# Kernel optimization log

Measured on AMD Instinct MI355X. Metric: run time of the kernel, lower is better.

The kernel has to match this reference:

```python
import jax, jax.numpy as jnp
import numpy as np

H = 200  # hidden size
D = 1    # input size
T = 8192 # sequence length


def setup_inputs() -> dict:
    key = jax.random.key(0)
    ks = jax.random.split(key, 11)
    s = 1.0 / np.sqrt(H)  # torch LSTM init scale
    u = lambda k, shape: jax.random.uniform(k, shape, jnp.float32, -s, s)
    return {
        "input_seq": jax.random.normal(ks[0], (T, D), jnp.float32),
        "W_ih0": u(ks[1], (4 * H, D)),
        "W_hh0": u(ks[2], (4 * H, H)),
        "b_ih0": u(ks[3], (4 * H,)),
        "b_hh0": u(ks[4], (4 * H,)),
        "W_ih1": u(ks[5], (4 * H, H)),
        "W_hh1": u(ks[6], (4 * H, H)),
        "b_ih1": u(ks[7], (4 * H,)),
        "b_hh1": u(ks[8], (4 * H,)),
        "W_out": u(ks[9], (D, H)),
        "b_out": u(ks[10], (D,)),
    }


def _cell(pre, h, c, Whh):
    # pre: [4H] = x @ W_ih.T + b_ih + b_hh already folded in
    g = pre + h @ Whh.T
    i, f, gg, o = jnp.split(g, 4)
    i = jax.nn.sigmoid(i)
    f = jax.nn.sigmoid(f)
    gg = jnp.tanh(gg)
    o = jax.nn.sigmoid(o)
    c = f * c + i * gg
    h = o * jnp.tanh(c)
    return h, c


def reference(input_seq, W_ih0, W_hh0, b_ih0, b_hh0,
              W_ih1, W_hh1, b_ih1, b_hh1, W_out, b_out):
    x = input_seq.reshape(input_seq.shape[0], -1)  # [T, D]
    # precompute layer-0 input projections for all timesteps (one big GEMM)
    pre0 = x @ W_ih0.T + (b_ih0 + b_hh0)           # [T, 4H]
    b1 = b_ih1 + b_hh1

    def step(carry, p0):
        h0, c0, h1, c1 = carry
        h0, c0 = _cell(p0, h0, c0, W_hh0)
        # eval mode: dropout(0.1) between layers is identity
        h1, c1 = _cell(h0 @ W_ih1.T + b1, h1, c1, W_hh1)
        return (h0, c0, h1, c1), None

    z = jnp.zeros((H,), x.dtype)
    (h0, c0, h1, c1), _ = jax.lax.scan(step, (z, z, z, z), pre0)
    # predictions[-1]: linear head on last top-layer hidden state -> [D]
    return h1 @ W_out.T + b_out
```

## Files before the change

### kernel.cpp

```cpp
#include <hip/hip_runtime.h>

#define TT 8192
#define HH 200
#define RD 1024
#define RDM 1023
#define BPWIN 900

typedef unsigned long long u64;
typedef unsigned int u32;
typedef _Float16 f16;
typedef _Float16 f16x2 __attribute__((ext_vector_type(2)));
typedef _Float16 half8 __attribute__((ext_vector_type(8)));
typedef float f32x4 __attribute__((ext_vector_type(4)));

__device__ __forceinline__ float sigmoidf_(float x){ return 1.0f/(1.0f+__expf(-x)); }
__device__ __forceinline__ float tanhf_(float x){
    float e = __expf(2.0f*fabsf(x));
    float r = 1.0f - 2.0f/(e + 1.0f);
    return copysignf(r, x);
}
__device__ __forceinline__ u64 pcku(u32 tag, u32 v){ return ((u64)tag<<32) | v; }
__device__ __forceinline__ u64 pckf(u32 tag, float v){ return pcku(tag, __float_as_uint(v)); }
__device__ __forceinline__ u64 ald(const u64* p){
    return __hip_atomic_load((u64*)p, __ATOMIC_RELAXED, __HIP_MEMORY_SCOPE_AGENT);
}
__device__ __forceinline__ void ast(u64* p, u64 v){
    __hip_atomic_store(p, v, __ATOMIC_RELAXED, __HIP_MEMORY_SCOPE_AGENT);
}
__device__ __forceinline__ u32 pkh(float a, float b){
    f16x2 v = { (f16)a, (f16)b };
    return __builtin_bit_cast(u32, v);
}
__device__ __forceinline__ float unpk(u32 u, int hi){
    f16x2 v = __builtin_bit_cast(f16x2, u);
    return (float)v[hi];
}
__device__ __forceinline__ float dot2(u32 a, u32 b, float c){
#if __has_builtin(__builtin_amdgcn_fdot2)
    return __builtin_amdgcn_fdot2(__builtin_bit_cast(f16x2, a),
                                  __builtin_bit_cast(f16x2, b), c, false);
#else
    f16x2 av = __builtin_bit_cast(f16x2, a), bv = __builtin_bit_cast(f16x2, b);
    return c + (float)av[0]*(float)bv[0] + (float)av[1]*(float)bv[1];
#endif
}
__device__ __forceinline__ u32 poll1u(const u64* p, u32 tag){
    u64 v = ald(p);
    while ((u32)(v >> 32) != tag) { __builtin_amdgcn_s_sleep(1); v = ald(p); }
    return (u32)v;
}
__device__ __forceinline__ void poll100(const u64* base, u32 tag, int l,
                                        u32* o0, u32* o1){
    const bool g1 = (l + 64 < 100);
    u64 v0, v1 = 0;
    for(;;){
        v0 = ald(base + l);
        if (g1) v1 = ald(base + l + 64);
        if ((u32)(v0>>32)==tag && (!g1 || (u32)(v1>>32)==tag)) break;
        __builtin_amdgcn_s_sleep(1);
    }
    *o0 = (u32)v0;
    *o1 = (u32)v1;
}

__global__ __launch_bounds__(512)
__attribute__((amdgpu_waves_per_eu(2, 2)))
void lstm_pipe(const float* __restrict__ x,
               const float* __restrict__ Wih0, const float* __restrict__ Whh0,
               const float* __restrict__ bih0, const float* __restrict__ bhh0,
               const float* __restrict__ Wih1, const float* __restrict__ Whh1,
               const float* __restrict__ bih1, const float* __restrict__ bhh1,
               const float* __restrict__ Wout, const float* __restrict__ bout,
               u64* __restrict__ hp0,
               u64* __restrict__ p1r,
               u32* __restrict__ prog,
               float* __restrict__ out)
{
    const int bid = blockIdx.x;
    const int tid = threadIdx.x;

    __shared__ float xs[TT];
    __shared__ __align__(16) u32 wl[10 * 7 * 64 * 4];
    __shared__ __align__(16) u32 hp_lds[2][112];
    __shared__ u32 hpbuf[2][100];
    __shared__ float s_pre[800];
    __shared__ float s_in[2][800];
    __shared__ __align__(16) float wbq[200][4];
    __shared__ __align__(16) float wbb[200][4];

    if (bid >= 2) {
        const int q = bid - 2;
        const int rl = tid >> 1, kh = tid & 1;
        const bool act = (tid < 400);
        u32 wp[50]; float bs = 0.f; int row = 0;
        if (act) {
            row = q * 200 + rl;
            const float* wr = Wih1 + (size_t)row * HH + kh * 100;
            #pragma unroll
            for (int i = 0; i < 50; ++i) wp[i] = pkh(wr[2*i], wr[2*i+1]);
            #pragma unroll
            for (int i = 0; i < 50; ++i) asm volatile("" : "+v"(wp[i]));
            if (kh == 0) bs = bih1[row] + bhh1[row];
        } else if (tid >= 448) {
            u32 o0, o1;
            poll100(hp0, 1u, tid - 448, &o0, &o1);
            hpbuf[0][tid - 448] = o0;
            if (tid - 448 + 64 < 100) hpbuf[0][tid - 448 + 64] = o1;
        }
        u32 prog_c = 0;
        __syncthreads();
        for (int t = 0; t < TT; ++t) {
            if (act) {
                const u32* hb = hpbuf[t & 1] + kh * 50;
                float a0 = 0.f, a1 = 0.f;
                #pragma unroll
                for (int i = 0; i < 50; i += 2) a0 = dot2(wp[i], hb[i], a0);
                #pragma unroll
                for (int i = 1; i < 50; i += 2) a1 = dot2(wp[i], hb[i], a1);
                float s = a0 + a1;
                s += __shfl_xor(s, 1);
                if (kh == 0)
                    ast(&p1r[(size_t)(t & RDM) * 800 + q * 200 + rl],
                        pckf((u32)(t + 1), s + bs));
            } else if (tid >= 448) {
                if (t + 1 < TT) {
                    u32 o0, o1;
                    poll100(&hp0[(size_t)(t + 1) * 100], (u32)(t + 2),
                            tid - 448, &o0, &o1);
                    hpbuf[(t + 1) & 1][tid - 448] = o0;
                    if (tid - 448 + 64 < 100) hpbuf[(t + 1) & 1][tid - 448 + 64] = o1;
                }
            } else if (tid == 440) {
                while ((int)(t + 1) - (int)prog_c >= BPWIN) {
                    __builtin_amdgcn_s_sleep(8);
                    prog_c = __hip_atomic_load(prog, __ATOMIC_RELAXED,
                                               __HIP_MEMORY_SCOPE_AGENT);
                }
            }
            __syncthreads();
        }
        return;
    }

    const int L = bid;
    const float* Whh = L ? Whh1 : Whh0;
    const int wv = tid >> 6, ln = tid & 63;
    const int lrow16 = ln & 15, lkgrp = ln >> 4;

    uint4 au[5][7];
    #pragma unroll
    for (int i = 0; i < 5; ++i) {
        const int row = 16 * (wv * 5 + i) + lrow16;
        const float* wr = Whh + (size_t)row * HH;
        #pragma unroll
        for (int kt = 0; kt < 7; ++kt) {
            const int kb = kt * 32 + lkgrp * 8;
            float w8[8];
            #pragma unroll
            for (int e = 0; e < 8; ++e) w8[e] = (kb + e < HH) ? wr[kb + e] : 0.f;
            au[i][kt] = make_uint4(pkh(w8[0],w8[1]), pkh(w8[2],w8[3]),
                                   pkh(w8[4],w8[5]), pkh(w8[6],w8[7]));
            asm volatile("" : "+v"(au[i][kt].x), "+v"(au[i][kt].y),
                              "+v"(au[i][kt].z), "+v"(au[i][kt].w));
        }
    }
    for (int idx = tid; idx < 10 * 7 * 64; idx += 512) {
        const int ti = idx / 448, rem = idx % 448;
        const int kt = rem / 64, l2 = rem & 63;
        const int row = 16 * (40 + ti) + (l2 & 15);
        const int kb = kt * 32 + (l2 >> 4) * 8;
        const float* wr = Whh + (size_t)row * HH;
        float w8[8];
        #pragma unroll
        for (int e = 0; e < 8; ++e) w8[e] = (kb + e < HH) ? wr[kb + e] : 0.f;
        *(uint4*)&wl[idx * 4] = make_uint4(pkh(w8[0],w8[1]), pkh(w8[2],w8[3]),
                                           pkh(w8[4],w8[5]), pkh(w8[6],w8[7]));
    }
    if (L == 0) {
        for (int i = tid; i < TT; i += 512) xs[i] = x[i];
        if (tid < 200) {
            #pragma unroll
            for (int q = 0; q < 4; ++q) {
                const int g = q * 200 + tid;
                wbq[tid][q] = Wih0[g];
                wbb[tid][q] = bih0[g] + bhh0[g];
            }
        }
    }
    if (tid < 112) { hp_lds[0][tid] = 0u; hp_lds[1][tid] = 0u; }

    if (L == 1 && wv >= 6) {
        const int lid = tid - 384;
        u64 v[7];
        for(;;){
            #pragma unroll
            for (int r = 0; r < 7; ++r) {
                const int s = lid + 128 * r;
                if (s < 800) v[r] = ald(&p1r[s]);
            }
            bool ok = true;
            #pragma unroll
            for (int r = 0; r < 7; ++r) {
                const int s = lid + 128 * r;
                if (s < 800 && (u32)(v[r]>>32) != 1u) ok = false;
            }
            if (ok) break;
            __builtin_amdgcn_s_sleep(1);
        }
        #pragma unroll
        for (int r = 0; r < 7; ++r) {
            const int s = lid + 128 * r;
            if (s < 800) s_in[0][s] = __uint_as_float((u32)v[r]);
        }
    }
    float cc = 0.f;
    __syncthreads();

    for (int t = 0; t < TT; ++t) {
        const int p = t & 1;
        f32x4 d0={0,0,0,0}, d1={0,0,0,0}, d2={0,0,0,0}, d3={0,0,0,0},
              d4={0,0,0,0}, e0={0,0,0,0}, e1={0,0,0,0};
        {
            const uint4* hp4 = (const uint4*)hp_lds[p];
            #pragma unroll
            for (int kt = 0; kt < 7; ++kt) {
                const half8 b = __builtin_bit_cast(half8, hp4[kt * 4 + lkgrp]);
                d0 = __builtin_amdgcn_mfma_f32_16x16x32_f16(
                         __builtin_bit_cast(half8, au[0][kt]), b, d0, 0, 0, 0);
                d1 = __builtin_amdgcn_mfma_f32_16x16x32_f16(
                         __builtin_bit_cast(half8, au[1][kt]), b, d1, 0, 0, 0);
                d2 = __builtin_amdgcn_mfma_f32_16x16x32_f16(
                         __builtin_bit_cast(half8, au[2][kt]), b, d2, 0, 0, 0);
                d3 = __builtin_amdgcn_mfma_f32_16x16x32_f16(
                         __builtin_bit_cast(half8, au[3][kt]), b, d3, 0, 0, 0);
                d4 = __builtin_amdgcn_mfma_f32_16x16x32_f16(
                         __builtin_bit_cast(half8, au[4][kt]), b, d4, 0, 0, 0);
                if (wv < 5) {
                    const uint4 a0 = *(const uint4*)
                        &wl[(((wv * 2 + 0) * 7 + kt) * 64 + ln) * 4];
                    const uint4 a1 = *(const uint4*)
                        &wl[(((wv * 2 + 1) * 7 + kt) * 64 + ln) * 4];
                    e0 = __builtin_amdgcn_mfma_f32_16x16x32_f16(
                             __builtin_bit_cast(half8, a0), b, e0, 0, 0, 0);
                    e1 = __builtin_amdgcn_mfma_f32_16x16x32_f16(
                             __builtin_bit_cast(half8, a1), b, e1, 0, 0, 0);
                }
            }
        }
        if (lrow16 == 0) {
            const int rb = 4 * lkgrp;
            *(float4*)&s_pre[16*(wv*5+0) + rb] = *(const float4*)&d0;
            *(float4*)&s_pre[16*(wv*5+1) + rb] = *(const float4*)&d1;
            *(float4*)&s_pre[16*(wv*5+2) + rb] = *(const float4*)&d2;
            *(float4*)&s_pre[16*(wv*5+3) + rb] = *(const float4*)&d3;
            *(float4*)&s_pre[16*(wv*5+4) + rb] = *(const float4*)&d4;
            if (wv < 5) {
                *(float4*)&s_pre[16*(40+wv*2+0) + rb] = *(const float4*)&e0;
                *(float4*)&s_pre[16*(40+wv*2+1) + rb] = *(const float4*)&e1;
            }
        }
        if (L == 1 && wv >= 6 && t + 1 < TT) {
            const int lid = tid - 384;
            const u64* slot = &p1r[(size_t)((t + 1) & RDM) * 800];
            const u32 tg = (u32)(t + 2);
            u64 v[7];
            for(;;){
                #pragma unroll
                for (int r = 0; r < 7; ++r) {
                    const int s = lid + 128 * r;
                    if (s < 800) v[r] = ald(slot + s);
                }
                bool ok = true;
                #pragma unroll
                for (int r = 0; r < 7; ++r) {
                    const int s = lid + 128 * r;
                    if (s < 800 && (u32)(v[r]>>32) != tg) ok = false;
                }
                if (ok) break;
                __builtin_amdgcn_s_sleep(1);
            }
            #pragma unroll
            for (int r = 0; r < 7; ++r) {
                const int s = lid + 128 * r;
                if (s < 800) s_in[(t + 1) & 1][s] = __uint_as_float((u32)v[r]);
            }
        }
        __syncthreads();
        if (tid < 200) {
            const int n = tid;
            float g0 = s_pre[n],       g1 = s_pre[200 + n],
                  g2 = s_pre[400 + n], g3 = s_pre[600 + n];
            if (L == 0) {
                const float xv = xs[t];
                const float4 w4 = *(const float4*)&wbq[n][0];
                const float4 b4 = *(const float4*)&wbb[n][0];
                g0 += xv*w4.x + b4.x; g1 += xv*w4.y + b4.y;
                g2 += xv*w4.z + b4.z; g3 += xv*w4.w + b4.w;
            } else {
                g0 += s_in[p][n];       g1 += s_in[p][200 + n];
                g2 += s_in[p][400 + n]; g3 += s_in[p][600 + n];
            }
            const float ig = sigmoidf_(g0), fg = sigmoidf_(g1);
            const float gg = tanhf_(g2),    og = sigmoidf_(g3);
            cc = fg * cc + ig * gg;
            const float h = og * tanhf_(cc);
            const float hq = __shfl_xor(h, 1);
            if (!(n & 1)) {
                const u32 pk = pkh(h, hq);
                hp_lds[p ^ 1][n >> 1] = pk;
                if (L == 0)
                    ast(&hp0[(size_t)t * 100 + (n >> 1)], pcku((u32)(t+1), pk));
            }
        } else if (L == 1 && tid == 200 && (t & 63) == 63) {
            __hip_atomic_store(prog, (u32)(t + 1), __ATOMIC_RELAXED,
                               __HIP_MEMORY_SCOPE_AGENT);
        }
        __syncthreads();
    }

    if (L == 1 && tid < 64) {
        const int fin = ((TT - 1) & 1) ^ 1;
        float s2 = 0.f;
        for (int k = tid; k < HH; k += 64)
            s2 += unpk(hp_lds[fin][k >> 1], k & 1) * Wout[k];
        #pragma unroll
        for (int off = 32; off > 0; off >>= 1) s2 += __shfl_down(s2, off);
        if (tid == 0) out[0] = s2 + bout[0];
    }
}

extern "C" void kernel_launch(void* const* d_in, const int* in_sizes, int n_in,
                              void* d_out, int out_size, void* d_ws, size_t ws_size,
                              hipStream_t stream) {
    const float* x    = (const float*)d_in[0];
    const float* Wih0 = (const float*)d_in[1];
    const float* Whh0 = (const float*)d_in[2];
    const float* bih0 = (const float*)d_in[3];
    const float* bhh0 = (const float*)d_in[4];
    const float* Wih1 = (const float*)d_in[5];
    const float* Whh1 = (const float*)d_in[6];
    const float* bih1 = (const float*)d_in[7];
    const float* bhh1 = (const float*)d_in[8];
    const float* Wout = (const float*)d_in[9];
    const float* bout = (const float*)d_in[10];
    float* out = (float*)d_out;

    char* ws = (char*)d_ws;
    u64* hp0  = (u64*)ws;
    u64* p1r  = (u64*)(ws + 6553600);
    u32* prog = (u32*)(ws + 13107200);

    hipMemsetAsync(ws, 0, 13107264, stream);

    hipLaunchKernelGGL(lstm_pipe, dim3(6), dim3(512), 0, stream,
        x, Wih0, Whh0, bih0, bhh0, Wih1, Whh1, bih1, bhh1, Wout, bout,
        hp0, p1r, prog, out);
}
```

Before: 16.01 ms.

## Keep Whh fragments in AGPRs, prefetch layer-1 inputs, use lighter LDS barriers

Whh tiles now stay in accumulator registers and feed MFMA through inline asm, which frees VGPRs. The layer-1 input polling moves off the matmul critical path into the activation phase, run by idle threads 256+, and the next slot is loaded one step ahead. __syncthreads is replaced with an s_barrier that waits only on LDS counters. The final head now reads a full-precision h buffer instead of unpacking fp16. Together these aim to shorten each serial timestep, at the risk of relying on weaker barrier semantics and hand-written asm constraints.

```diff
diff --git a/kernel.cpp b/kernel.cpp
--- a/kernel.cpp
+++ b/kernel.cpp
@@ -5,12 +5,13 @@
 #define RD 1024
 #define RDM 1023
 #define BPWIN 900
+#define NT 5
 
 typedef unsigned long long u64;
 typedef unsigned int u32;
 typedef _Float16 f16;
 typedef _Float16 f16x2 __attribute__((ext_vector_type(2)));
-typedef _Float16 half8 __attribute__((ext_vector_type(8)));
+typedef u32 u32x4 __attribute__((ext_vector_type(4)));
 typedef float f32x4 __attribute__((ext_vector_type(4)));
 
 __device__ __forceinline__ float sigmoidf_(float x){ return 1.0f/(1.0f+__expf(-x)); }
@@ -30,10 +31,6 @@
 __device__ __forceinline__ u32 pkh(float a, float b){
     f16x2 v = { (f16)a, (f16)b };
     return __builtin_bit_cast(u32, v);
-}
-__device__ __forceinline__ float unpk(u32 u, int hi){
-    f16x2 v = __builtin_bit_cast(f16x2, u);
-    return (float)v[hi];
 }
 __device__ __forceinline__ float dot2(u32 a, u32 b, float c){
 #if __has_builtin(__builtin_amdgcn_fdot2)
@@ -43,6 +40,18 @@
     f16x2 av = __builtin_bit_cast(f16x2, a), bv = __builtin_bit_cast(f16x2, b);
     return c + (float)av[0]*(float)bv[0] + (float)av[1]*(float)bv[1];
 #endif
+}
+__device__ __forceinline__ void mfma_a(f32x4& d, const u32x4& a, const u32x4& b){
+    asm("v_mfma_f32_16x16x32_f16 %0, %1, %2, %0" : "+v"(d) : "a"(a), "v"(b));
+}
+__device__ __forceinline__ void mfma_v(f32x4& d, const u32x4& a, const u32x4& b){
+    asm("v_mfma_f32_16x16x32_f16 %0, %1, %2, %0" : "+v"(d) : "v"(a), "v"(b));
+}
+__device__ __forceinline__ void bar_lds(){
+    __builtin_amdgcn_sched_barrier(0);
+    asm volatile("s_waitcnt lgkmcnt(0)" ::: "memory");
+    __builtin_amdgcn_s_barrier();
+    __builtin_amdgcn_sched_barrier(0);
 }
 __device__ __forceinline__ u32 poll1u(const u64* p, u32 tag){
     u64 v = ald(p);
@@ -87,6 +96,7 @@
     __shared__ float s_in[2][800];
     __shared__ __align__(16) float wbq[200][4];
     __shared__ __align__(16) float wbb[200][4];
+    __shared__ float h32[HH];
 
     if (bid >= 2) {
         const int q = bid - 2;
@@ -137,7 +147,7 @@
                                                __HIP_MEMORY_SCOPE_AGENT);
                 }
             }
-            __syncthreads();
+            bar_lds();
         }
         return;
     }
@@ -147,10 +157,10 @@
     const int wv = tid >> 6, ln = tid & 63;
     const int lrow16 = ln & 15, lkgrp = ln >> 4;
 
-    uint4 au[5][7];
+    u32x4 au[NT][7];
     #pragma unroll
-    for (int i = 0; i < 5; ++i) {
-        const int row = 16 * (wv * 5 + i) + lrow16;
+    for (int i = 0; i < NT; ++i) {
+        const int row = 16 * (wv * NT + i) + lrow16;
         const float* wr = Whh + (size_t)row * HH;
         #pragma unroll
         for (int kt = 0; kt < 7; ++kt) {
@@ -158,23 +168,22 @@
             float w8[8];
             #pragma unroll
             for (int e = 0; e < 8; ++e) w8[e] = (kb + e < HH) ? wr[kb + e] : 0.f;
-            au[i][kt] = make_uint4(pkh(w8[0],w8[1]), pkh(w8[2],w8[3]),
-                                   pkh(w8[4],w8[5]), pkh(w8[6],w8[7]));
-            asm volatile("" : "+v"(au[i][kt].x), "+v"(au[i][kt].y),
-                              "+v"(au[i][kt].z), "+v"(au[i][kt].w));
+            au[i][kt] = (u32x4){pkh(w8[0],w8[1]), pkh(w8[2],w8[3]),
+                                pkh(w8[4],w8[5]), pkh(w8[6],w8[7])};
+            asm volatile("" : "+a"(au[i][kt]));
         }
     }
     for (int idx = tid; idx < 10 * 7 * 64; idx += 512) {
         const int ti = idx / 448, rem = idx % 448;
-        const int kt = rem / 64, l2 = rem & 63;
-        const int row = 16 * (40 + ti) + (l2 & 15);
-        const int kb = kt * 32 + (l2 >> 4) * 8;
+        const int kt = rem / 64, l2i = rem & 63;
+        const int row = 16 * (40 + ti) + (l2i & 15);
+        const int kb = kt * 32 + (l2i >> 4) * 8;
         const float* wr = Whh + (size_t)row * HH;
         float w8[8];
         #pragma unroll
         for (int e = 0; e < 8; ++e) w8[e] = (kb + e < HH) ? wr[kb + e] : 0.f;
-        *(uint4*)&wl[idx * 4] = make_uint4(pkh(w8[0],w8[1]), pkh(w8[2],w8[3]),
-                                           pkh(w8[4],w8[5]), pkh(w8[6],w8[7]));
+        *(u32x4*)&wl[idx * 4] = (u32x4){pkh(w8[0],w8[1]), pkh(w8[2],w8[3]),
+                                        pkh(w8[4],w8[5]), pkh(w8[6],w8[7])};
     }
     if (L == 0) {
         for (int i = tid; i < TT; i += 512) xs[i] = x[i];
@@ -188,29 +197,20 @@
         }
     }
     if (tid < 112) { hp_lds[0][tid] = 0u; hp_lds[1][tid] = 0u; }
-
-    if (L == 1 && wv >= 6) {
-        const int lid = tid - 384;
-        u64 v[7];
-        for(;;){
-            #pragma unroll
-            for (int r = 0; r < 7; ++r) {
-                const int s = lid + 128 * r;
-                if (s < 800) v[r] = ald(&p1r[s]);
-            }
-            bool ok = true;
-            #pragma unroll
-            for (int r = 0; r < 7; ++r) {
-                const int s = lid + 128 * r;
-                if (s < 800 && (u32)(v[r]>>32) != 1u) ok = false;
-            }
-            if (ok) break;
-            __builtin_amdgcn_s_sleep(1);
-        }
-        #pragma unroll
-        for (int r = 0; r < 7; ++r) {
-            const int s = lid + 128 * r;
-            if (s < 800) s_in[0][s] = __uint_as_float((u32)v[r]);
+    if (tid < HH) h32[tid] = 0.f;
+
+    const int l2 = tid - 256;
+    u64 rv[4] = {0, 0, 0, 0};
+    if (L == 1 && tid >= 256) {
+        #pragma unroll
+        for (int r = 0; r < 4; ++r) {
+            const int s = l2 + 256 * r;
+            if (s < 800) s_in[0][s] = __uint_as_float(poll1u(&p1r[s], 1u));
+        }
+        #pragma unroll
+        for (int r = 0; r < 4; ++r) {
+            const int s = l2 + 256 * r;
+            if (s < 800) rv[r] = ald(&p1r[800 + s]);
         }
     }
     float cc = 0.f;
@@ -218,74 +218,43 @@
 
     for (int t = 0; t < TT; ++t) {
         const int p = t & 1;
-        f32x4 d0={0,0,0,0}, d1={0,0,0,0}, d2={0,0,0,0}, d3={0,0,0,0},
-              d4={0,0,0,0}, e0={0,0,0,0}, e1={0,0,0,0};
         {
-            const uint4* hp4 = (const uint4*)hp_lds[p];
+            f32x4 d0={0.f,0.f,0.f,0.f}, d1={0.f,0.f,0.f,0.f},
+                  d2={0.f,0.f,0.f,0.f}, d3={0.f,0.f,0.f,0.f},
+                  d4={0.f,0.f,0.f,0.f}, e0={0.f,0.f,0.f,0.f},
+                  e1={0.f,0.f,0.f,0.f};
+            const u32* hp = hp_lds[p];
             #pragma unroll
             for (int kt = 0; kt < 7; ++kt) {
-                const half8 b = __builtin_bit_cast(half8, hp4[kt * 4 + lkgrp]);
-                d0 = __builtin_amdgcn_mfma_f32_16x16x32_f16(
-                         __builtin_bit_cast(half8, au[0][kt]), b, d0, 0, 0, 0);
-                d1 = __builtin_amdgcn_mfma_f32_16x16x32_f16(
-                         __builtin_bit_cast(half8, au[1][kt]), b, d1, 0, 0, 0);
-                d2 = __builtin_amdgcn_mfma_f32_16x16x32_f16(
-                         __builtin_bit_cast(half8, au[2][kt]), b, d2, 0, 0, 0);
-                d3 = __builtin_amdgcn_mfma_f32_16x16x32_f16(
-                         __builtin_bit_cast(half8, au[3][kt]), b, d3, 0, 0, 0);
-                d4 = __builtin_amdgcn_mfma_f32_16x16x32_f16(
-                         __builtin_bit_cast(half8, au[4][kt]), b, d4, 0, 0, 0);
+                const u32x4 b = *(const u32x4*)&hp[(kt * 4 + lkgrp) * 4];
+                mfma_a(d0, au[0][kt], b);
+                mfma_a(d1, au[1][kt], b);
+                mfma_a(d2, au[2][kt], b);
+                mfma_a(d3, au[3][kt], b);
+                mfma_a(d4, au[4][kt], b);
                 if (wv < 5) {
-                    const uint4 a0 = *(const uint4*)
+                    const u32x4 a0 = *(const u32x4*)
                         &wl[(((wv * 2 + 0) * 7 + kt) * 64 + ln) * 4];
-                    const uint4 a1 = *(const uint4*)
+                    const u32x4 a1 = *(const u32x4*)
                         &wl[(((wv * 2 + 1) * 7 + kt) * 64 + ln) * 4];
-                    e0 = __builtin_amdgcn_mfma_f32_16x16x32_f16(
-                             __builtin_bit_cast(half8, a0), b, e0, 0, 0, 0);
-                    e1 = __builtin_amdgcn_mfma_f32_16x16x32_f16(
-                             __builtin_bit_cast(half8, a1), b, e1, 0, 0, 0);
-                }
-            }
-        }
-        if (lrow16 == 0) {
-            const int rb = 4 * lkgrp;
-            *(float4*)&s_pre[16*(wv*5+0) + rb] = *(const float4*)&d0;
-            *(float4*)&s_pre[16*(wv*5+1) + rb] = *(const float4*)&d1;
-            *(float4*)&s_pre[16*(wv*5+2) + rb] = *(const float4*)&d2;
-            *(float4*)&s_pre[16*(wv*5+3) + rb] = *(const float4*)&d3;
-            *(float4*)&s_pre[16*(wv*5+4) + rb] = *(const float4*)&d4;
-            if (wv < 5) {
-                *(float4*)&s_pre[16*(40+wv*2+0) + rb] = *(const float4*)&e0;
-                *(float4*)&s_pre[16*(40+wv*2+1) + rb] = *(const float4*)&e1;
-            }
-        }
-        if (L == 1 && wv >= 6 && t + 1 < TT) {
-            const int lid = tid - 384;
-            const u64* slot = &p1r[(size_t)((t + 1) & RDM) * 800];
-            const u32 tg = (u32)(t + 2);
-            u64 v[7];
-            for(;;){
-                #pragma unroll
-                for (int r = 0; r < 7; ++r) {
-                    const int s = lid + 128 * r;
-                    if (s < 800) v[r] = ald(slot + s);
-                }
-                bool ok = true;
-                #pragma unroll
-                for (int r = 0; r < 7; ++r) {
-                    const int s = lid + 128 * r;
-                    if (s < 800 && (u32)(v[r]>>32) != tg) ok = false;
-                }
-                if (ok) break;
-                __builtin_amdgcn_s_sleep(1);
-            }
-            #pragma unroll
-            for (int r = 0; r < 7; ++r) {
-                const int s = lid + 128 * r;
-                if (s < 800) s_in[(t + 1) & 1][s] = __uint_as_float((u32)v[r]);
-            }
-        }
-        __syncthreads();
+                    mfma_v(e0, a0, b);
+                    mfma_v(e1, a1, b);
+                }
+            }
+            if (lrow16 == 0) {
+                const int rb = 4 * lkgrp;
+                *(f32x4*)&s_pre[16*(wv*NT+0) + rb] = d0;
+                *(f32x4*)&s_pre[16*(wv*NT+1) + rb] = d1;
+                *(f32x4*)&s_pre[16*(wv*NT+2) + rb] = d2;
+                *(f32x4*)&s_pre[16*(wv*NT+3) + rb] = d3;
+                *(f32x4*)&s_pre[16*(wv*NT+4) + rb] = d4;
+                if (wv < 5) {
+                    *(f32x4*)&s_pre[16*(40+wv*2+0) + rb] = e0;
+                    *(f32x4*)&s_pre[16*(40+wv*2+1) + rb] = e1;
+                }
+            }
+        }
+        bar_lds();
         if (tid < 200) {
             const int n = tid;
             float g0 = s_pre[n],       g1 = s_pre[200 + n],
@@ -304,6 +273,7 @@
             const float gg = tanhf_(g2),    og = sigmoidf_(g3);
             cc = fg * cc + ig * gg;
             const float h = og * tanhf_(cc);
+            h32[n] = h;
             const float hq = __shfl_xor(h, 1);
             if (!(n & 1)) {
                 const u32 pk = pkh(h, hq);
@@ -311,18 +281,41 @@
                 if (L == 0)
                     ast(&hp0[(size_t)t * 100 + (n >> 1)], pcku((u32)(t+1), pk));
             }
+        } else if (L == 1 && tid >= 256) {
+            if (t + 1 < TT) {
+                const u32 tg = (u32)(t + 2);
+                const u64* slot = &p1r[(size_t)((t + 1) & RDM) * 800];
+                #pragma unroll
+                for (int r = 0; r < 4; ++r) {
+                    const int s = l2 + 256 * r;
+                    if (s < 800) {
+                        u64 v = rv[r];
+                        while ((u32)(v >> 32) != tg) {
+                            __builtin_amdgcn_s_sleep(1);
+                            v = ald(slot + s);
+                        }
+                        s_in[(t + 1) & 1][s] = __uint_as_float((u32)v);
+                    }
+                }
+            }
+            if (t + 2 < TT) {
+                const u64* slot2 = &p1r[(size_t)((t + 2) & RDM) * 800];
+                #pragma unroll
+                for (int r = 0; r < 4; ++r) {
+                    const int s = l2 + 256 * r;
+                    if (s < 800) rv[r] = ald(slot2 + s);
+                }
+            }
         } else if (L == 1 && tid == 200 && (t & 63) == 63) {
             __hip_atomic_store(prog, (u32)(t + 1), __ATOMIC_RELAXED,
                                __HIP_MEMORY_SCOPE_AGENT);
         }
-        __syncthreads();
+        bar_lds();
     }
 
     if (L == 1 && tid < 64) {
-        const int fin = ((TT - 1) & 1) ^ 1;
         float s2 = 0.f;
-        for (int k = tid; k < HH; k += 64)
-            s2 += unpk(hp_lds[fin][k >> 1], k & 1) * Wout[k];
+        for (int k = tid; k < HH; k += 64) s2 += h32[k] * Wout[k];
         #pragma unroll
         for (int off = 32; off > 0; off >>= 1) s2 += __shfl_down(s2, off);
         if (tid == 0) out[0] = s2 + bout[0];
```

Result: faster. 13.39 ms (-16.3%).
